# Optimization experiments

Measured on AMD Instinct MI355X. Metric: run time of the kernel, lower is better.

Reference implementation:

```python
import jax, jax.numpy as jnp
import numpy as np

T = 1024          # tokens (batch*seq, vLLM flattened layout)
D = 2048          # hidden_size
H = 16            # attention heads
HD = D // H       # head_dim = 128
E = 16            # num routed experts
K = 2             # top_k
IM = 1408         # moe_intermediate_size
IS = 5632         # shared_expert_intermediate_size
EPS = 1e-6
THETA = 10000.0


def setup_inputs() -> dict:
    key = jax.random.key(0)
    ks = jax.random.split(key, 14)
    s = 0.02  # weight scale
    n = jax.random.normal
    return {
        "positions": jnp.arange(T, dtype=jnp.int32),
        "hidden_states": n(ks[0], (T, D), jnp.float32),
        "ln1_w": 1.0 + s * n(ks[1], (D,), jnp.float32),
        "ln2_w": 1.0 + s * n(ks[2], (D,), jnp.float32),
        "qkv_w": s * n(ks[3], (D, 3 * H * HD), jnp.float32),
        "qkv_b": s * n(ks[4], (3 * H * HD,), jnp.float32),
        "o_w": s * n(ks[5], (H * HD, D), jnp.float32),
        "router_w": s * n(ks[6], (D, E), jnp.float32),
        "w_gate": s * n(ks[7], (E, D, IM), jnp.float32),
        "w_up": s * n(ks[8], (E, D, IM), jnp.float32),
        "w_down": s * n(ks[9], (E, IM, D), jnp.float32),
        "sh_gate_up": s * n(ks[10], (D, 2 * IS), jnp.float32),
        "sh_down": s * n(ks[11], (IS, D), jnp.float32),
        "sh_expert_gate": s * n(ks[12], (D, 1), jnp.float32),
    }


def _rmsnorm(x, w):
    var = jnp.mean(x * x, axis=-1, keepdims=True)
    return x * jax.lax.rsqrt(var + EPS) * w


def _rope(x, positions):
    # neox-style rotary: x [T, H, HD]
    half = HD // 2
    inv_freq = 1.0 / (THETA ** (jnp.arange(0, half, dtype=jnp.float32) / half * 1.0))
    inv_freq = 1.0 / (THETA ** (jnp.arange(0, HD, 2, dtype=jnp.float32) / HD))
    ang = positions.astype(jnp.float32)[:, None] * inv_freq  # [T, HD/2]
    cos = jnp.cos(ang)[:, None, :]
    sin = jnp.sin(ang)[:, None, :]
    x1, x2 = x[..., :half], x[..., half:]
    return jnp.concatenate([x1 * cos - x2 * sin, x2 * cos + x1 * sin], axis=-1)


def reference(positions, hidden_states, ln1_w, ln2_w, qkv_w, qkv_b, o_w,
              router_w, w_gate, w_up, w_down, sh_gate_up, sh_down,
              sh_expert_gate):
    # --- input RMSNorm (residual=None path) ---
    residual = hidden_states
    x = _rmsnorm(hidden_states, ln1_w)

    # --- self-attention: QKV + RoPE + causal SDPA + o_proj ---
    qkv = x @ qkv_w + qkv_b
    q, k, v = jnp.split(qkv, [H * HD, 2 * H * HD], axis=-1)
    q = _rope(q.reshape(T, H, HD), positions)
    k = _rope(k.reshape(T, H, HD), positions)
    v = v.reshape(T, H, HD)
    scale = HD ** -0.5
    scores = jnp.einsum('thd,shd->hts', q, k) * scale  # [H, T, T]
    causal = jnp.tril(jnp.ones((T, T), dtype=bool))
    scores = jnp.where(causal[None], scores, jnp.finfo(scores.dtype).min)
    attn = jax.nn.softmax(scores, axis=-1)
    ctx = jnp.einsum('hts,shd->thd', attn, v).reshape(T, H * HD)
    attn_out = ctx @ o_w

    # --- fused add + post-attention RMSNorm ---
    residual = residual + attn_out
    x = _rmsnorm(residual, ln2_w)

    # --- sparse MoE: router -> softmax -> top-k (renormalized) -> experts ---
    logits = x @ router_w                                    # [T, E]
    probs = jax.nn.softmax(logits.astype(jnp.float32), axis=-1)
    topv, topi = jax.lax.top_k(probs, K)                     # [T, K]
    topv = topv / jnp.sum(topv, axis=-1, keepdims=True)      # norm_topk_prob
    w = jnp.zeros((T, E), dtype=x.dtype).at[
        jnp.arange(T)[:, None], topi].set(topv.astype(x.dtype))
    g = jax.nn.silu(jnp.einsum('td,edi->tei', x, w_gate)) * \
        jnp.einsum('td,edi->tei', x, w_up)                   # [T, E, IM]
    moe_out = jnp.einsum('tei,eid,te->td', g, w_down, w)

    # --- shared expert with sigmoid gate ---
    gu = x @ sh_gate_up
    g2, u2 = jnp.split(gu, 2, axis=-1)
    shared = (jax.nn.silu(g2) * u2) @ sh_down
    shared = jax.nn.sigmoid(x @ sh_expert_gate) * shared

    hidden_states = moe_out + shared
    return hidden_states, residual
```

## Files before the change

### kernel.cpp

```cpp
#include <hip/hip_runtime.h>

constexpr int T_  = 1024;
constexpr int D_  = 2048;
constexpr int H_  = 16;
constexpr int HD_ = 128;
constexpr int E_  = 16;
constexpr int IM_ = 1408;
constexpr int IS_ = 5632;

typedef __attribute__((ext_vector_type(8))) short bf16x8;
typedef __attribute__((ext_vector_type(4))) short short4v;
typedef __attribute__((ext_vector_type(4))) float f32x4;

__device__ __forceinline__ short f2bf(float f){
  unsigned u = __builtin_bit_cast(unsigned, f);
  u += 0x7fffu + ((u >> 16) & 1u);
  return (short)(u >> 16);
}
__device__ __forceinline__ float bf2f(short s){
  unsigned u = ((unsigned)(unsigned short)s) << 16;
  return __builtin_bit_cast(float, u);
}
__device__ __forceinline__ unsigned cvtpk(float lo, float hi){
  unsigned r;
  asm("v_cvt_pk_bf16_f32 %0, %1, %2" : "=v"(r) : "v"(lo), "v"(hi));
  return r;
}
__device__ __forceinline__ float pk_lo(unsigned h){
  return __builtin_bit_cast(float, h << 16);
}
__device__ __forceinline__ float pk_hi(unsigned h){
  return __builtin_bit_cast(float, h & 0xffff0000u);
}
__device__ __forceinline__ f32x4 mfma16(bf16x8 a, bf16x8 b, f32x4 c){
  return __builtin_amdgcn_mfma_f32_16x16x32_bf16(a, b, c, 0, 0, 0);
}
__device__ __forceinline__ void split3(float f, short& h, short& m, short& l){
  h = f2bf(f); float r = f - bf2f(h);
  m = f2bf(r); l = f2bf(r - bf2f(m));
}
__device__ __forceinline__ void split2(float f, short& h, short& m){
  h = f2bf(f); m = f2bf(f - bf2f(h));
}
__device__ __forceinline__ uint4 mk4(unsigned a, unsigned b, unsigned c, unsigned d){
  uint4 r; r.x=a; r.y=b; r.z=c; r.w=d; return r;
}
#define LGKM0_BAR() do{ asm volatile("s_waitcnt lgkmcnt(0)" ::: "memory"); \
                        __builtin_amdgcn_s_barrier(); }while(0)

__global__ __launch_bounds__(256) void sctab_kernel(
    const int* __restrict__ pos, float* __restrict__ cst, float* __restrict__ snt)
{
  int idx = blockIdx.x * 256 + threadIdx.x;
  if (idx >= T_ * 64) return;
  int t = idx >> 6, i = idx & 63;
  float invf = (float)pow(10000.0, -(double)i / 64.0);
  float ang  = (float)pos[t] * invf;
  double s, c;
  sincos((double)ang, &s, &c);
  cst[idx] = (float)c; snt[idx] = (float)s;
}

__global__ __launch_bounds__(256) void rms_kernel(
    const float* __restrict__ x, const float* __restrict__ w,
    short* __restrict__ o0, short* __restrict__ o1, short* __restrict__ o2,
    short* __restrict__ ob, float* __restrict__ of)
{
  int t = blockIdx.x, tid = threadIdx.x;
  const float* xr = x + (size_t)t * D_;
  float4 va = ((const float4*)xr)[tid*2];
  float4 vb = ((const float4*)xr)[tid*2+1];
  float ss = va.x*va.x + va.y*va.y + va.z*va.z + va.w*va.w
           + vb.x*vb.x + vb.y*vb.y + vb.z*vb.z + vb.w*vb.w;
  for (int o = 32; o; o >>= 1) ss += __shfl_xor(ss, o, 64);
  __shared__ float red[4];
  int lane = tid & 63, wid = tid >> 6;
  if (lane == 0) red[wid] = ss;
  __syncthreads();
  ss = red[0] + red[1] + red[2] + red[3];
  float rs = 1.0f / sqrtf(ss * (1.0f/D_) + 1e-6f);
  float4 wa = ((const float4*)w)[tid*2];
  float4 wb = ((const float4*)w)[tid*2+1];
  float xv[8] = {va.x,va.y,va.z,va.w, vb.x,vb.y,vb.z,vb.w};
  float wv[8] = {wa.x,wa.y,wa.z,wa.w, wb.x,wb.y,wb.z,wb.w};
  size_t base = (size_t)t * D_ + tid*8;
  #pragma unroll
  for (int p = 0; p < 4; ++p){
    float f0 = xv[2*p]   * rs * wv[2*p];
    float f1 = xv[2*p+1] * rs * wv[2*p+1];
    if (o0){
      unsigned h = cvtpk(f0, f1);
      float r0 = f0 - pk_lo(h), r1 = f1 - pk_hi(h);
      unsigned m = cvtpk(r0, r1);
      unsigned l = cvtpk(r0 - pk_lo(m), r1 - pk_hi(m));
      *(unsigned*)&o0[base + 2*p] = h;
      *(unsigned*)&o1[base + 2*p] = m;
      *(unsigned*)&o2[base + 2*p] = l;
    }
    if (ob) *(unsigned*)&ob[base + 2*p] = cvtpk(f0, f1);
    if (of){ of[base + 2*p] = f0; of[base + 2*p + 1] = f1; }
  }
}

__global__ __launch_bounds__(256) void prepk_kernel(
    const float* __restrict__ qkv, const float* __restrict__ cst,
    const float* __restrict__ snt, short* __restrict__ Kp0, short* __restrict__ Kp1)
{
  int idx = blockIdx.x * 256 + threadIdx.x;
  int c = idx & 7, t = (idx >> 3) & (T_-1), h = idx >> 13;
  int d0 = c * 8;
  const float* kp = qkv + (size_t)t * (3*D_) + D_ + h*HD_;
  const float* cp = cst + t*64 + d0;
  const float* sp = snt + t*64 + d0;
  unsigned lh[4], ll[4], hh[4], hl[4];
  #pragma unroll
  for (int p = 0; p < 4; ++p){
    float xl0 = kp[d0+2*p],    xh0 = kp[d0+64+2*p];
    float xl1 = kp[d0+2*p+1],  xh1 = kp[d0+64+2*p+1];
    float cv0 = cp[2*p], sv0 = sp[2*p], cv1 = cp[2*p+1], sv1 = sp[2*p+1];
    float rl0 = xl0*cv0 - xh0*sv0, rh0 = xh0*cv0 + xl0*sv0;
    float rl1 = xl1*cv1 - xh1*sv1, rh1 = xh1*cv1 + xl1*sv1;
    unsigned a = cvtpk(rl0, rl1);
    ll[p] = cvtpk(rl0 - pk_lo(a), rl1 - pk_hi(a)); lh[p] = a;
    unsigned b = cvtpk(rh0, rh1);
    hl[p] = cvtpk(rh0 - pk_lo(b), rh1 - pk_hi(b)); hh[p] = b;
  }
  size_t ob = ((size_t)h*T_ + t) * HD_;
  *(uint4*)(Kp0 + ob + d0)      = mk4(lh[0],lh[1],lh[2],lh[3]);
  *(uint4*)(Kp0 + ob + 64 + d0) = mk4(hh[0],hh[1],hh[2],hh[3]);
  *(uint4*)(Kp1 + ob + d0)      = mk4(ll[0],ll[1],ll[2],ll[3]);
  *(uint4*)(Kp1 + ob + 64 + d0) = mk4(hl[0],hl[1],hl[2],hl[3]);
}

__global__ __launch_bounds__(256) void prepv_kernel(
    const float* __restrict__ qkv, short* __restrict__ Vp0, short* __restrict__ Vp1)
{
  __shared__ short Vl[2][128][72];
  int t0 = blockIdx.x * 64, h = blockIdx.y, tid = threadIdx.x;
  int r = tid >> 2, cq = (tid & 3) * 32;
  const float* src = qkv + (size_t)(t0+r) * (3*D_) + 2*D_ + h*HD_ + cq;
  #pragma unroll
  for (int jj = 0; jj < 8; ++jj){
    float4 v = *(const float4*)(src + jj*4);
    float vv[4] = {v.x, v.y, v.z, v.w};
    #pragma unroll
    for (int u = 0; u < 4; ++u){
      int d = cq + jj*4 + u;
      short a, b; split2(vv[u], a, b);
      Vl[0][d][r] = a; Vl[1][d][r] = b;
    }
  }
  __syncthreads();
  int d = tid >> 1, tc = (tid & 1) * 32;
  short* dst0 = Vp0 + ((size_t)h*HD_ + d) * T_ + t0 + tc;
  short* dst1 = Vp1 + ((size_t)h*HD_ + d) * T_ + t0 + tc;
  #pragma unroll
  for (int q = 0; q < 4; ++q){
    *(uint4*)(dst0 + q*8) = *(const uint4*)&Vl[0][d][tc + q*8];
    *(uint4*)(dst1 + q*8) = *(const uint4*)&Vl[1][d][tc + q*8];
  }
}

__global__ __launch_bounds__(256) void prepw_kernel(
    const float* __restrict__ w, short* __restrict__ P0, short* __restrict__ P1)
{
  __shared__ short L0[64][72], L1[64][72];
  int k0 = blockIdx.x * 64, n0 = blockIdx.y * 64;
  int tid = threadIdx.x;
  int r = tid >> 2, cq = (tid & 3) * 16;
  const float* src = w + (size_t)(k0 + r) * D_ + n0 + cq;
  #pragma unroll
  for (int q = 0; q < 4; ++q){
    float4 f = *(const float4*)(src + q*4);
    float fv[4] = {f.x, f.y, f.z, f.w};
    #pragma unroll
    for (int u = 0; u < 4; ++u){
      int n = cq + q*4 + u;
      short a, b; split2(fv[u], a, b);
      L0[n][r] = a; L1[n][r] = b;
    }
  }
  __syncthreads();
  int n = tid >> 2, kq = (tid & 3) * 16;
  short* d0 = P0 + (size_t)(n0 + n) * D_ + k0 + kq;
  short* d1 = P1 + (size_t)(n0 + n) * D_ + k0 + kq;
  *(uint4*)(d0)     = *(const uint4*)&L0[n][kq];
  *(uint4*)(d0 + 8) = *(const uint4*)&L0[n][kq + 8];
  *(uint4*)(d1)     = *(const uint4*)&L1[n][kq];
  *(uint4*)(d1 + 8) = *(const uint4*)&L1[n][kq + 8];
}

__global__ __launch_bounds__(128) void attn_kernel(
    const float* __restrict__ qkv,
    const float* __restrict__ cst, const float* __restrict__ snt,
    const short* __restrict__ Kp0, const short* __restrict__ Kp1,
    const short* __restrict__ Vp0, const short* __restrict__ Vp1,
    short* __restrict__ c0p, short* __restrict__ c1p, short* __restrict__ c2p)
{
  __shared__ __attribute__((aligned(16))) short Ks[2][2][32][128];
  __shared__ __attribute__((aligned(16))) short Vs[2][2][128][40];
  __shared__ __attribute__((aligned(16))) short Ps[3][2][16][40];

  const float SCALE = 0.08838834764831845f;
  const int QW = 3*D_;
  int h = blockIdx.x;
  int ys = blockIdx.y;
  int qt = (ys < 16) ? (ys*2) : ((31-ys)*2 + 1);
  int q0 = qt * 32;
  int tid = threadIdx.x, lane = tid & 63, wq = tid >> 6;
  int lr = lane & 15, kq8 = (lane >> 4) * 8, r4 = (lane >> 4) * 4;

  bf16x8 qfh[4], qfm[4], qfl[4];
  { int qrow = q0 + wq*16 + lr;
    const float* qp = qkv + (size_t)qrow * QW + h*HD_;
    const float* cp = cst + qrow*64;
    const float* sp = snt + qrow*64;
    float x[4][8], cs[2][8], sn[2][8], rot[4][8];
    for (int ks = 0; ks < 4; ++ks)
      for (int j = 0; j < 8; ++j) x[ks][j] = qp[ks*32 + kq8 + j];
    for (int hf = 0; hf < 2; ++hf)
      for (int j = 0; j < 8; ++j){
        cs[hf][j] = cp[hf*32 + kq8 + j];
        sn[hf][j] = sp[hf*32 + kq8 + j];
      }
    for (int j = 0; j < 8; ++j){
      rot[0][j] = x[0][j]*cs[0][j] - x[2][j]*sn[0][j];
      rot[1][j] = x[1][j]*cs[1][j] - x[3][j]*sn[1][j];
      rot[2][j] = x[2][j]*cs[0][j] + x[0][j]*sn[0][j];
      rot[3][j] = x[3][j]*cs[1][j] + x[1][j]*sn[1][j];
    }
    for (int ks = 0; ks < 4; ++ks)
      for (int j = 0; j < 8; ++j){
        short a, b, c; split3(rot[ks][j], a, b, c);
        qfh[ks][j] = a; qfm[ks][j] = b; qfl[ks][j] = c;
      }
  }

  f32x4 acc[8];
  for (int i = 0; i < 8; ++i) acc[i] = f32x4{0.f,0.f,0.f,0.f};
  float mrun[4] = {-1e30f,-1e30f,-1e30f,-1e30f};
  float lrun[4] = {0.f,0.f,0.f,0.f};

  int krow = tid >> 2, kc = (tid & 3) * 32;
  const short* kb0 = Kp0 + ((size_t)h*T_ + krow) * HD_ + kc;
  const short* kb1 = Kp1 + ((size_t)h*T_ + krow) * HD_ + kc;
  const short* vb0 = Vp0 + ((size_t)h*HD_ + tid) * T_;
  const short* vb1 = Vp1 + ((size_t)h*HD_ + tid) * T_;
  int xr = (krow & 7) * 8;

  uint4 kr0[4], kr1[4], vr0[4], vr1[4];
  auto LOAD = [&](int it){
    size_t ko = (size_t)it * 32 * HD_;
    const uint4* p0 = (const uint4*)(kb0 + ko);
    const uint4* p1 = (const uint4*)(kb1 + ko);
    #pragma unroll
    for (int g = 0; g < 4; ++g){ kr0[g] = p0[g]; kr1[g] = p1[g]; }
    const uint4* q0p = (const uint4*)(vb0 + it*32);
    const uint4* q1p = (const uint4*)(vb1 + it*32);
    #pragma unroll
    for (int g = 0; g < 4; ++g){ vr0[g] = q0p[g]; vr1[g] = q1p[g]; }
  };
  auto STORE = [&](int buf){
    #pragma unroll
    for (int g = 0; g < 4; ++g){
      int col = (kc + 8*g) ^ xr;
      *(uint4*)&Ks[buf][0][krow][col] = kr0[g];
      *(uint4*)&Ks[buf][1][krow][col] = kr1[g];
    }
    #pragma unroll
    for (int g = 0; g < 4; ++g){
      *(uint4*)&Vs[buf][0][tid][g*8] = vr0[g];
      *(uint4*)&Vs[buf][1][tid][g*8] = vr1[g];
    }
  };

  int nt = qt + 1;
  LOAD(0); STORE(0);
  if (nt > 1) LOAD(1);
  LGKM0_BAR();

  int cur = 0;
  for (int it = 0; it < nt; ++it){
    if (it + 1 < nt){
      STORE(cur ^ 1);
      if (it + 2 < nt) LOAD(it + 2);
    }
    int kv0 = it * 32;
    int xl = (lr & 7) * 8;
    f32x4 s0 = f32x4{0.f,0.f,0.f,0.f}, s1 = f32x4{0.f,0.f,0.f,0.f};
    #pragma unroll
    for (int ks = 0; ks < 4; ++ks){
      int col = (ks*32 + kq8) ^ xl;
      bf16x8 b0h = *(const bf16x8*)&Ks[cur][0][lr][col];
      bf16x8 b0m = *(const bf16x8*)&Ks[cur][1][lr][col];
      bf16x8 b1h = *(const bf16x8*)&Ks[cur][0][16+lr][col];
      bf16x8 b1m = *(const bf16x8*)&Ks[cur][1][16+lr][col];
      s0 = mfma16(qfh[ks], b0h, s0); s0 = mfma16(qfh[ks], b0m, s0);
      s0 = mfma16(qfm[ks], b0h, s0); s0 = mfma16(qfm[ks], b0m, s0);
      s0 = mfma16(qfl[ks], b0h, s0);
      s1 = mfma16(qfh[ks], b1h, s1); s1 = mfma16(qfh[ks], b1m, s1);
      s1 = mfma16(qfm[ks], b1h, s1); s1 = mfma16(qfm[ks], b1m, s1);
      s1 = mfma16(qfl[ks], b1h, s1);
    }
    float pm[2][4]; float alpha[4];
    for (int r = 0; r < 4; ++r){
      int qr = q0 + wq*16 + r4 + r;
      float x0 = s0[r]*SCALE, x1 = s1[r]*SCALE;
      if (kv0 + lr > qr)      x0 = -1e30f;
      if (kv0 + 16 + lr > qr) x1 = -1e30f;
      float mt_ = fmaxf(x0, x1);
      mt_ = fmaxf(mt_, __shfl_xor(mt_, 1, 64));
      mt_ = fmaxf(mt_, __shfl_xor(mt_, 2, 64));
      mt_ = fmaxf(mt_, __shfl_xor(mt_, 4, 64));
      mt_ = fmaxf(mt_, __shfl_xor(mt_, 8, 64));
      float mn = fmaxf(mrun[r], mt_);
      float p0 = __expf(x0 - mn), p1 = __expf(x1 - mn);
      pm[0][r] = p0; pm[1][r] = p1;
      float ls = p0 + p1;
      ls += __shfl_xor(ls, 1, 64); ls += __shfl_xor(ls, 2, 64);
      ls += __shfl_xor(ls, 4, 64); ls += __shfl_xor(ls, 8, 64);
      alpha[r] = __expf(mrun[r] - mn);
      lrun[r] = lrun[r]*alpha[r] + ls;
      mrun[r] = mn;
    }
    for (int dt = 0; dt < 8; ++dt){
      f32x4 a = acc[dt];
      a[0]*=alpha[0]; a[1]*=alpha[1]; a[2]*=alpha[2]; a[3]*=alpha[3];
      acc[dt] = a;
    }
    for (int nn = 0; nn < 2; ++nn)
      for (int r = 0; r < 4; ++r){
        short a, b, c; split3(pm[nn][r], a, b, c);
        Ps[0][wq][r4+r][nn*16+lr] = a;
        Ps[1][wq][r4+r][nn*16+lr] = b;
        Ps[2][wq][r4+r][nn*16+lr] = c;
      }
    bf16x8 pah = *(const bf16x8*)&Ps[0][wq][lr][kq8];
    bf16x8 pam = *(const bf16x8*)&Ps[1][wq][lr][kq8];
    bf16x8 pal = *(const bf16x8*)&Ps[2][wq][lr][kq8];
    #pragma unroll
    for (int dt = 0; dt < 8; ++dt){
      bf16x8 vbh = *(const bf16x8*)&Vs[cur][0][dt*16+lr][kq8];
      bf16x8 vbm = *(const bf16x8*)&Vs[cur][1][dt*16+lr][kq8];
      acc[dt] = mfma16(pah, vbh, acc[dt]);
      acc[dt] = mfma16(pah, vbm, acc[dt]);
      acc[dt] = mfma16(pam, vbh, acc[dt]);
      acc[dt] = mfma16(pam, vbm, acc[dt]);
      acc[dt] = mfma16(pal, vbh, acc[dt]);
    }
    LGKM0_BAR();
    cur ^= 1;
  }
  for (int dt = 0; dt < 8; ++dt)
    for (int r = 0; r < 4; ++r){
      int qr = q0 + wq*16 + r4 + r;
      float o = acc[dt][r] / lrun[r];
      size_t ix = (size_t)qr * D_ + h*HD_ + dt*16 + lr;
      short a, b, c; split3(o, a, b, c);
      c0p[ix] = a; c1p[ix] = b; c2p[ix] = c;
    }
}

enum { M_QKV = 0, M_OPROJ = 1 };

template<int MODE>
__global__ __launch_bounds__(256) void gemm3_kernel(
    const short* __restrict__ A0, const short* __restrict__ A1, const short* __restrict__ A2,
    const float* __restrict__ Bw,
    const short* __restrict__ Bp0, const short* __restrict__ Bp1,
    const float* __restrict__ bias, const float* __restrict__ addsrc,
    float* __restrict__ outF,
    int K, int lda, int ldb, int ldo)
{
  __shared__ __attribute__((aligned(16))) short As[2][3][64][40];
  __shared__ __attribute__((aligned(16))) short Bs[2][2][64][40];

  int m0 = blockIdx.y * 64, n0 = blockIdx.x * 64;
  int tid = threadIdx.x, lane = tid & 63, wid = tid >> 6;
  int wm = wid >> 1, wn = wid & 1;
  int lr = lane & 15, kq8 = (lane >> 4) * 8;

  f32x4 acc[2][2];
  for (int i = 0; i < 2; ++i)
    for (int j = 0; j < 2; ++j) acc[i][j] = f32x4{0.f,0.f,0.f,0.f};

  int arow = tid >> 2, ac = (tid & 3) * 8;
  const short* aP0 = A0 + (size_t)(m0 + arow) * lda + ac;
  const short* aP1 = A1 + (size_t)(m0 + arow) * lda + ac;
  const short* aP2 = A2 + (size_t)(m0 + arow) * lda + ac;
  int bn = tid & 63, bk0 = (tid >> 6) * 8;
  const float* bP  = Bw  ? (Bw + n0 + bn) : nullptr;
  const short* bq0 = Bp0 ? (Bp0 + (size_t)(n0 + bn) * K) : nullptr;
  const short* bq1 = Bp1 ? (Bp1 + (size_t)(n0 + bn) * K) : nullptr;

  uint4 ar0_0, ar1_0, ar2_0, ar0_1, ar1_1, ar2_1;
  float br_0[8], br_1[8];
  uint4 pb0_0, pb1_0, pb0_1, pb1_1;

  auto LOAD0 = [&](int kt){
    ar0_0 = *(const uint4*)(aP0 + kt*32);
    ar1_0 = *(const uint4*)(aP1 + kt*32);
    ar2_0 = *(const uint4*)(aP2 + kt*32);
    if constexpr (MODE == M_QKV){
      const float* p = bP + (size_t)(kt*32 + bk0) * ldb;
      #pragma unroll
      for (int j = 0; j < 8; ++j) br_0[j] = p[(size_t)j * ldb];
    } else {
      pb0_0 = *(const uint4*)(bq0 + kt*32 + bk0);
      pb1_0 = *(const uint4*)(bq1 + kt*32 + bk0);
    }
  };
  auto LOAD1 = [&](int kt){
    ar0_1 = *(const uint4*)(aP0 + kt*32);
    ar1_1 = *(const uint4*)(aP1 + kt*32);
    ar2_1 = *(const uint4*)(aP2 + kt*32);
    if constexpr (MODE == M_QKV){
      const float* p = bP + (size_t)(kt*32 + bk0) * ldb;
      #pragma unroll
      for (int j = 0; j < 8; ++j) br_1[j] = p[(size_t)j * ldb];
    } else {
      pb0_1 = *(const uint4*)(bq0 + kt*32 + bk0);
      pb1_1 = *(const uint4*)(bq1 + kt*32 + bk0);
    }
  };
  auto STORE0 = [&](int buf){
    *(uint4*)&As[buf][0][arow][ac] = ar0_0;
    *(uint4*)&As[buf][1][arow][ac] = ar1_0;
    *(uint4*)&As[buf][2][arow][ac] = ar2_0;
    if constexpr (MODE == M_QKV){
      unsigned hh[4], mm[4];
      #pragma unroll
      for (int p = 0; p < 4; ++p){
        unsigned h = cvtpk(br_0[2*p], br_0[2*p+1]);
        mm[p] = cvtpk(br_0[2*p] - pk_lo(h), br_0[2*p+1] - pk_hi(h));
        hh[p] = h;
      }
      *(uint4*)&Bs[buf][0][bn][bk0] = mk4(hh[0],hh[1],hh[2],hh[3]);
      *(uint4*)&Bs[buf][1][bn][bk0] = mk4(mm[0],mm[1],mm[2],mm[3]);
    } else {
      *(uint4*)&Bs[buf][0][bn][bk0] = pb0_0;
      *(uint4*)&Bs[buf][1][bn][bk0] = pb1_0;
    }
  };
  auto STORE1 = [&](int buf){
    *(uint4*)&As[buf][0][arow][ac] = ar0_1;
    *(uint4*)&As[buf][1][arow][ac] = ar1_1;
    *(uint4*)&As[buf][2][arow][ac] = ar2_1;
    if constexpr (MODE == M_QKV){
      unsigned hh[4], mm[4];
      #pragma unroll
      for (int p = 0; p < 4; ++p){
        unsigned h = cvtpk(br_1[2*p], br_1[2*p+1]);
        mm[p] = cvtpk(br_1[2*p] - pk_lo(h), br_1[2*p+1] - pk_hi(h));
        hh[p] = h;
      }
      *(uint4*)&Bs[buf][0][bn][bk0] = mk4(hh[0],hh[1],hh[2],hh[3]);
      *(uint4*)&Bs[buf][1][bn][bk0] = mk4(mm[0],mm[1],mm[2],mm[3]);
    } else {
      *(uint4*)&Bs[buf][0][bn][bk0] = pb0_1;
      *(uint4*)&Bs[buf][1][bn][bk0] = pb1_1;
    }
  };
  auto COMPUTE = [&](int cur){
    bf16x8 aH[2], aM[2], aL[2];
    #pragma unroll
    for (int mt = 0; mt < 2; ++mt){
      aH[mt] = *(const bf16x8*)&As[cur][0][wm*32 + mt*16 + lr][kq8];
      aM[mt] = *(const bf16x8*)&As[cur][1][wm*32 + mt*16 + lr][kq8];
      aL[mt] = *(const bf16x8*)&As[cur][2][wm*32 + mt*16 + lr][kq8];
    }
    #pragma unroll
    for (int nt = 0; nt < 2; ++nt){
      bf16x8 bH = *(const bf16x8*)&Bs[cur][0][wn*32 + nt*16 + lr][kq8];
      bf16x8 bM = *(const bf16x8*)&Bs[cur][1][wn*32 + nt*16 + lr][kq8];
      #pragma unroll
      for (int mt = 0; mt < 2; ++mt){
        f32x4 a = acc[mt][nt];
        a = mfma16(aH[mt], bH, a);
        a = mfma16(aH[mt], bM, a);
        a = mfma16(aM[mt], bH, a);
        a = mfma16(aM[mt], bM, a);
        a = mfma16(aL[mt], bH, a);
        acc[mt][nt] = a;
      }
    }
  };

  int NK = K / 32;
  LOAD0(0); LOAD1(1);
  STORE0(0);
  LOAD0(2);
  LGKM0_BAR();

  int cur = 0;
  for (int kt = 0; kt < NK; kt += 2){
    if (kt + 1 < NK) STORE1(cur ^ 1);
    if (kt + 3 < NK) LOAD1(kt + 3);
    COMPUTE(cur);
    LGKM0_BAR();
    cur ^= 1;
    if (kt + 1 < NK){
      if (kt + 2 < NK) STORE0(cur ^ 1);
      if (kt + 4 < NK) LOAD0(kt + 4);
      COMPUTE(cur);
      LGKM0_BAR();
      cur ^= 1;
    }
  }

  for (int mt = 0; mt < 2; ++mt)
    for (int nt = 0; nt < 2; ++nt)
      for (int r = 0; r < 4; ++r){
        int mrow = m0 + wm*32 + mt*16 + (lane >> 4)*4 + r;
        int col  = n0 + wn*32 + nt*16 + lr;
        float v = acc[mt][nt][r];
        if constexpr (MODE == M_QKV){
          outF[(size_t)mrow * ldo + col] = v + bias[col];
        } else {
          outF[(size_t)mrow * ldo + col] = v + addsrc[(size_t)mrow * ldo + col];
        }
      }
}

__global__ __launch_bounds__(256) void gu_kernel(
    const short* __restrict__ x2b,
    const float* __restrict__ w_gate, const float* __restrict__ w_up,
    const float* __restrict__ sh_gu,
    short* __restrict__ gbuf, short* __restrict__ sbuf,
    const int* __restrict__ perm, const int* __restrict__ offE,
    const int* __restrict__ cntE)
{
  __shared__ __attribute__((aligned(16))) short As[2][128][40];
  __shared__ __attribute__((aligned(16))) short Bs[2][2][64][40];

  int z = blockIdx.z;
  bool SH = (z == E_);
  int N    = SH ? IS_ : IM_;
  int n0 = blockIdx.x * 64;
  if (n0 >= N) return;
  int mcnt  = SH ? T_ : cntE[z];
  int mbase = SH ? 0  : offE[z];
  int m0 = blockIdx.y * 128;
  if (m0 >= mcnt) return;
  int ldb = SH ? 2*IS_ : IM_;
  int ldo = SH ? IS_   : IM_;
  const float* Bg = SH ? sh_gu         : (w_gate + (size_t)z * D_ * IM_);
  const float* Bu = SH ? (sh_gu + IS_) : (w_up   + (size_t)z * D_ * IM_);
  short* outB = SH ? sbuf : gbuf;

  int tid = threadIdx.x, lane = tid & 63, wid = tid >> 6;
  int wm = wid >> 1, wn = wid & 1;
  int lr = lane & 15, kq8 = (lane >> 4) * 8;

  f32x4 acc0[4][2], acc1[4][2];
  #pragma unroll
  for (int i = 0; i < 4; ++i)
    for (int j = 0; j < 2; ++j){
      acc0[i][j] = f32x4{0.f,0.f,0.f,0.f};
      acc1[i][j] = f32x4{0.f,0.f,0.f,0.f};
    }

  int arow = tid >> 1, acol = (tid & 1) * 16;
  int aRowIdx;
  { int mr = m0 + arow;
    int mc = (mr < mcnt) ? mr : 0;
    aRowIdx = SH ? mc : perm[mbase + mc];
  }
  const short* aP = x2b + (size_t)aRowIdx * D_;

  int bn_ = tid & 63, bkq = (tid >> 6) * 8;
  const float* bP0 = Bg + n0 + bn_;
  const float* bP1 = Bu + n0 + bn_;

  uint4 arA_0, arB_0, arA_1, arB_1;
  float br0_0[8], br1_0[8], br0_1[8], br1_1[8];

  auto LOAD0 = [&](int kt){
    const uint4* s = (const uint4*)(aP + kt*32 + acol);
    arA_0 = s[0]; arB_0 = s[1];
    const float* p0 = bP0 + (size_t)(kt*32 + bkq) * ldb;
    const float* p1 = bP1 + (size_t)(kt*32 + bkq) * ldb;
    #pragma unroll
    for (int j = 0; j < 8; ++j){ br0_0[j] = p0[(size_t)j * ldb]; br1_0[j] = p1[(size_t)j * ldb]; }
  };
  auto LOAD1 = [&](int kt){
    const uint4* s = (const uint4*)(aP + kt*32 + acol);
    arA_1 = s[0]; arB_1 = s[1];
    const float* p0 = bP0 + (size_t)(kt*32 + bkq) * ldb;
    const float* p1 = bP1 + (size_t)(kt*32 + bkq) * ldb;
    #pragma unroll
    for (int j = 0; j < 8; ++j){ br0_1[j] = p0[(size_t)j * ldb]; br1_1[j] = p1[(size_t)j * ldb]; }
  };
  auto STORE0 = [&](int buf){
    *(uint4*)&As[buf][arow][acol]   = arA_0;
    *(uint4*)&As[buf][arow][acol+8] = arB_0;
    unsigned v0[4], v1[4];
    #pragma unroll
    for (int p = 0; p < 4; ++p){
      v0[p] = cvtpk(br0_0[2*p], br0_0[2*p+1]);
      v1[p] = cvtpk(br1_0[2*p], br1_0[2*p+1]);
    }
    *(uint4*)&Bs[buf][0][bn_][bkq] = mk4(v0[0],v0[1],v0[2],v0[3]);
    *(uint4*)&Bs[buf][1][bn_][bkq] = mk4(v1[0],v1[1],v1[2],v1[3]);
  };
  auto STORE1 = [&](int buf){
    *(uint4*)&As[buf][arow][acol]   = arA_1;
    *(uint4*)&As[buf][arow][acol+8] = arB_1;
    unsigned v0[4], v1[4];
    #pragma unroll
    for (int p = 0; p < 4; ++p){
      v0[p] = cvtpk(br0_1[2*p], br0_1[2*p+1]);
      v1[p] = cvtpk(br1_1[2*p], br1_1[2*p+1]);
    }
    *(uint4*)&Bs[buf][0][bn_][bkq] = mk4(v0[0],v0[1],v0[2],v0[3]);
    *(uint4*)&Bs[buf][1][bn_][bkq] = mk4(v1[0],v1[1],v1[2],v1[3]);
  };
  auto COMPUTE = [&](int cur){
    bf16x8 a[4];
    #pragma unroll
    for (int mt = 0; mt < 4; ++mt)
      a[mt] = *(const bf16x8*)&As[cur][wm*64 + mt*16 + lr][kq8];
    #pragma unroll
    for (int nt = 0; nt < 2; ++nt){
      int nrow = wn*32 + nt*16 + lr;
      bf16x8 b0 = *(const bf16x8*)&Bs[cur][0][nrow][kq8];
      bf16x8 b1 = *(const bf16x8*)&Bs[cur][1][nrow][kq8];
      #pragma unroll
      for (int mt = 0; mt < 4; ++mt){
        acc0[mt][nt] = mfma16(a[mt], b0, acc0[mt][nt]);
        acc1[mt][nt] = mfma16(a[mt], b1, acc1[mt][nt]);
      }
    }
  };

  constexpr int NK = D_ / 32;
  LOAD0(0); LOAD1(1);
  STORE0(0);
  LOAD0(2);
  LGKM0_BAR();

  int cur = 0;
  for (int kt = 0; kt < NK; kt += 2){
    if (kt + 1 < NK) STORE1(cur ^ 1);
    if (kt + 3 < NK) LOAD1(kt + 3);
    COMPUTE(cur);
    LGKM0_BAR();
    cur ^= 1;
    if (kt + 2 < NK) STORE0(cur ^ 1);
    if (kt + 4 < NK) LOAD0(kt + 4);
    COMPUTE(cur);
    LGKM0_BAR();
    cur ^= 1;
  }

  for (int mt = 0; mt < 4; ++mt)
    for (int nt = 0; nt < 2; ++nt)
      for (int r = 0; r < 4; ++r){
        int mrow = m0 + wm*64 + mt*16 + (lane >> 4)*4 + r;
        if (mrow >= mcnt) continue;
        int col = n0 + wn*32 + nt*16 + lr;
        float v = acc0[mt][nt][r];
        float u = acc1[mt][nt][r];
        float sv = v / (1.f + __expf(-v)) * u;
        outB[(size_t)(mbase + mrow) * ldo + col] = f2bf(sv);
      }
}

__global__ __launch_bounds__(256) void dn_kernel(
    const short* __restrict__ gbuf, const short* __restrict__ sbuf,
    const float* __restrict__ w_down, const float* __restrict__ sh_down,
    float* __restrict__ outF,
    const int* __restrict__ perm, const int* __restrict__ offE,
    const int* __restrict__ cntE, const float* __restrict__ wgt,
    const float* __restrict__ sig)
{
  __shared__ __attribute__((aligned(16))) short As[2][128][40];
  __shared__ __attribute__((aligned(16))) short Bs[2][64][40];

  int z = blockIdx.z;
  bool SH = (z == E_);
  int K = SH ? IS_ : IM_;
  int mcnt  = SH ? T_ : cntE[z];
  int mbase = SH ? 0  : offE[z];
  int m0 = blockIdx.y * 128;
  if (m0 >= mcnt) return;
  int n0 = blockIdx.x * 64;
  const float* Bq = SH ? sh_down : (w_down + (size_t)z * IM_ * D_);
  const short* Ab = SH ? sbuf : gbuf;

  int tid = threadIdx.x, lane = tid & 63, wid = tid >> 6;
  int wm = wid >> 1, wn = wid & 1;
  int lr = lane & 15, kq8 = (lane >> 4) * 8;

  f32x4 acc0[4][2];
  #pragma unroll
  for (int i = 0; i < 4; ++i)
    for (int j = 0; j < 2; ++j) acc0[i][j] = f32x4{0.f,0.f,0.f,0.f};

  int arow = tid >> 1, acol = (tid & 1) * 16;
  int mr = m0 + arow;
  int mc = (mr < mcnt) ? mr : 0;
  const short* aP = Ab + (size_t)(SH ? mc : (mbase + mc)) * K;

  int bn_ = tid & 63, bkq = (tid >> 6) * 8;
  const float* bP0 = Bq + n0 + bn_;

  uint4 arA_0, arB_0, arA_1, arB_1;
  float br_0[8], br_1[8];

  auto LOAD0 = [&](int kt){
    const uint4* s = (const uint4*)(aP + kt*32 + acol);
    arA_0 = s[0]; arB_0 = s[1];
    const float* p0 = bP0 + (size_t)(kt*32 + bkq) * D_;
    #pragma unroll
    for (int j = 0; j < 8; ++j) br_0[j] = p0[(size_t)j * D_];
  };
  auto LOAD1 = [&](int kt){
    const uint4* s = (const uint4*)(aP + kt*32 + acol);
    arA_1 = s[0]; arB_1 = s[1];
    const float* p0 = bP0 + (size_t)(kt*32 + bkq) * D_;
    #pragma unroll
    for (int j = 0; j < 8; ++j) br_1[j] = p0[(size_t)j * D_];
  };
  auto STORE0 = [&](int buf){
    *(uint4*)&As[buf][arow][acol]   = arA_0;
    *(uint4*)&As[buf][arow][acol+8] = arB_0;
    unsigned v0[4];
    #pragma unroll
    for (int p = 0; p < 4; ++p) v0[p] = cvtpk(br_0[2*p], br_0[2*p+1]);
    *(uint4*)&Bs[buf][bn_][bkq] = mk4(v0[0],v0[1],v0[2],v0[3]);
  };
  auto STORE1 = [&](int buf){
    *(uint4*)&As[buf][arow][acol]   = arA_1;
    *(uint4*)&As[buf][arow][acol+8] = arB_1;
    unsigned v0[4];
    #pragma unroll
    for (int p = 0; p < 4; ++p) v0[p] = cvtpk(br_1[2*p], br_1[2*p+1]);
    *(uint4*)&Bs[buf][bn_][bkq] = mk4(v0[0],v0[1],v0[2],v0[3]);
  };
  auto COMPUTE = [&](int cur){
    bf16x8 a[4];
    #pragma unroll
    for (int mt = 0; mt < 4; ++mt)
      a[mt] = *(const bf16x8*)&As[cur][wm*64 + mt*16 + lr][kq8];
    #pragma unroll
    for (int nt = 0; nt < 2; ++nt){
      bf16x8 b0 = *(const bf16x8*)&Bs[cur][wn*32 + nt*16 + lr][kq8];
      #pragma unroll
      for (int mt = 0; mt < 4; ++mt)
        acc0[mt][nt] = mfma16(a[mt], b0, acc0[mt][nt]);
    }
  };

  int NK = K / 32;
  LOAD0(0); LOAD1(1);
  STORE0(0);
  LOAD0(2);
  LGKM0_BAR();

  int cur = 0;
  for (int kt = 0; kt < NK; kt += 2){
    if (kt + 1 < NK) STORE1(cur ^ 1);
    if (kt + 3 < NK) LOAD1(kt + 3);
    COMPUTE(cur);
    LGKM0_BAR();
    cur ^= 1;
    if (kt + 2 < NK) STORE0(cur ^ 1);
    if (kt + 4 < NK) LOAD0(kt + 4);
    COMPUTE(cur);
    LGKM0_BAR();
    cur ^= 1;
  }

  for (int mt = 0; mt < 4; ++mt)
    for (int nt = 0; nt < 2; ++nt)
      for (int r = 0; r < 4; ++r){
        int mrow = m0 + wm*64 + mt*16 + (lane >> 4)*4 + r;
        if (mrow >= mcnt) continue;
        int col = n0 + wn*32 + nt*16 + lr;
        float v = acc0[mt][nt][r];
        if (SH){
          atomicAdd(&outF[(size_t)mrow * D_ + col], sig[mrow] * v);
        } else {
          int tk = perm[mbase + mrow];
          atomicAdd(&outF[(size_t)tk * D_ + col], v * wgt[mbase + mrow]);
        }
      }
}

__global__ __launch_bounds__(256) void router_kernel(
    const float* __restrict__ x2f, const float* __restrict__ rw,
    const float* __restrict__ seg, int* __restrict__ te, float* __restrict__ tw,
    float* __restrict__ sig, int* __restrict__ cnt)
{
  int t = blockIdx.x, tid = threadIdx.x, lane = tid & 63, w = tid >> 6;
  const float* xr = x2f + (size_t)t * D_;
  float a0 = 0.f, a1 = 0.f, a2 = 0.f, a3 = 0.f, ag = 0.f;
  for (int j = 0; j < 32; ++j){
    int d = lane + 64*j;
    float xv = xr[d];
    const float* rp = rw + (size_t)d * E_ + w*4;
    a0 += xv * rp[0]; a1 += xv * rp[1]; a2 += xv * rp[2]; a3 += xv * rp[3];
    ag += xv * seg[d];
  }
  for (int o = 32; o; o >>= 1){
    a0 += __shfl_xor(a0, o, 64); a1 += __shfl_xor(a1, o, 64);
    a2 += __shfl_xor(a2, o, 64); a3 += __shfl_xor(a3, o, 64);
    ag += __shfl_xor(ag, o, 64);
  }
  __shared__ float lg[16];
  __shared__ float sgv;
  if (lane == 0){
    lg[w*4+0] = a0; lg[w*4+1] = a1; lg[w*4+2] = a2; lg[w*4+3] = a3;
    if (w == 0) sgv = ag;
  }
  __syncthreads();
  if (tid == 0){
    int e0 = 0; float v0 = lg[0];
    for (int ee = 1; ee < 16; ++ee) if (lg[ee] > v0){ v0 = lg[ee]; e0 = ee; }
    int e1 = -1; float v1 = -3e38f;
    for (int ee = 0; ee < 16; ++ee){
      if (ee == e0) continue;
      if (lg[ee] > v1){ v1 = lg[ee]; e1 = ee; }
    }
    float w0 = 1.f / (1.f + expf(v1 - v0));
    te[2*t] = e0; te[2*t+1] = e1;
    tw[2*t] = w0; tw[2*t+1] = 1.f - w0;
    atomicAdd(&cnt[e0], 1); atomicAdd(&cnt[e1], 1);
    sig[t] = 1.f / (1.f + expf(-sgv));
  }
}

__global__ void prefix_kernel(const int* __restrict__ cnt, int* __restrict__ offE,
                              int* __restrict__ cursor)
{
  if (threadIdx.x == 0){
    int s = 0;
    for (int e = 0; e < 16; ++e){ offE[e] = s; s += cnt[e]; }
  }
  if (threadIdx.x < 16) cursor[threadIdx.x] = 0;
}

__global__ __launch_bounds__(256) void scatter_kernel(
    const int* __restrict__ te, const float* __restrict__ tw,
    const int* __restrict__ offE, int* __restrict__ cursor,
    int* __restrict__ perm, float* __restrict__ wgt)
{
  int t = blockIdx.x * 256 + threadIdx.x;
  if (t >= T_) return;
  for (int i = 0; i < 2; ++i){
    int e = te[2*t + i];
    int pos = offE[e] + atomicAdd(&cursor[e], 1);
    perm[pos] = t; wgt[pos] = tw[2*t + i];
  }
}

extern "C" void kernel_launch(void* const* d_in, const int* in_sizes, int n_in,
                              void* d_out, int out_size, void* d_ws, size_t ws_size,
                              hipStream_t stream)
{
  const int*   positions = (const int*)  d_in[0];
  const float* hidden    = (const float*)d_in[1];
  const float* ln1       = (const float*)d_in[2];
  const float* ln2       = (const float*)d_in[3];
  const float* qkv_w     = (const float*)d_in[4];
  const float* qkv_b     = (const float*)d_in[5];
  const float* o_w       = (const float*)d_in[6];
  const float* router_w  = (const float*)d_in[7];
  const float* w_gate    = (const float*)d_in[8];
  const float* w_up      = (const float*)d_in[9];
  const float* w_down    = (const float*)d_in[10];
  const float* sh_gu     = (const float*)d_in[11];
  const float* sh_down   = (const float*)d_in[12];
  const float* sh_eg     = (const float*)d_in[13];

  float* out_hidden = (float*)d_out;
  float* out_resid  = (float*)d_out + (size_t)T_ * D_;

  char* wp = (char*)d_ws;
  auto alloc = [&](size_t b){ char* p = wp; wp += (b + 255) & ~(size_t)255; return p; };

  float* qkv  = (float*)alloc((size_t)T_ * 3*D_ * 4);
  short* x1h  = (short*)alloc((size_t)T_ * D_ * 2);
  short* x1m  = (short*)alloc((size_t)T_ * D_ * 2);
  short* x1l  = (short*)alloc((size_t)T_ * D_ * 2);
  short* Kp0  = (short*)alloc((size_t)T_ * D_ * 2);
  short* Kp1  = (short*)alloc((size_t)T_ * D_ * 2);
  short* Vp0  = (short*)alloc((size_t)T_ * D_ * 2);
  short* Vp1  = (short*)alloc((size_t)T_ * D_ * 2);
  float* cst  = (float*)alloc((size_t)T_ * 64 * 4);
  float* snt  = (float*)alloc((size_t)T_ * 64 * 4);
  int*   te   = (int*)  alloc(2*T_*4);
  float* tw   = (float*)alloc(2*T_*4);
  float* sig  = (float*)alloc(T_*4);
  int*   cnt    = (int*)alloc(256);
  int*   offE   = (int*)alloc(256);
  int*   cursor = (int*)alloc(256);
  int*   perm = (int*)  alloc(2*T_*4);
  float* wgt  = (float*)alloc(2*T_*4);

  short* ctxh = x1h;
  short* ctxm = x1m;
  short* ctxl = x1l;
  float* x2f  = qkv;
  short* sbuf = (short*)((char*)qkv + (size_t)8388608);
  short* gbuf = (short*)x1h;
  short* x2b  = (short*)((char*)x1h + (size_t)5767168);
  short* Wo0  = Kp0;
  short* Wo1  = Vp0;

  hipMemsetAsync(cnt, 0, 64, stream);
  hipMemsetAsync(out_hidden, 0, (size_t)T_ * D_ * 4, stream);

  sctab_kernel<<<(T_*64)/256, 256, 0, stream>>>(positions, cst, snt);

  rms_kernel<<<T_, 256, 0, stream>>>(hidden, ln1, x1h, x1m, x1l, nullptr, nullptr);

  gemm3_kernel<M_QKV><<<dim3(96, 16), 256, 0, stream>>>(
      x1h, x1m, x1l, qkv_w, nullptr, nullptr, qkv_b, nullptr, qkv,
      D_, D_, 3*D_, 3*D_);

  prepk_kernel<<<(T_*H_*8)/256, 256, 0, stream>>>(qkv, cst, snt, Kp0, Kp1);
  prepv_kernel<<<dim3(16, 16), 256, 0, stream>>>(qkv, Vp0, Vp1);

  attn_kernel<<<dim3(16, 32), 128, 0, stream>>>(
      qkv, cst, snt, Kp0, Kp1, Vp0, Vp1, ctxh, ctxm, ctxl);

  prepw_kernel<<<dim3(32, 32), 256, 0, stream>>>(o_w, Wo0, Wo1);

  gemm3_kernel<M_OPROJ><<<dim3(32, 16), 256, 0, stream>>>(
      ctxh, ctxm, ctxl, nullptr, Wo0, Wo1, nullptr, hidden, out_resid,
      D_, D_, D_, D_);

  rms_kernel<<<T_, 256, 0, stream>>>(out_resid, ln2, nullptr, nullptr, nullptr, x2b, x2f);

  router_kernel<<<T_, 256, 0, stream>>>(x2f, router_w, sh_eg, te, tw, sig, cnt);
  prefix_kernel<<<1, 64, 0, stream>>>(cnt, offE, cursor);
  scatter_kernel<<<4, 256, 0, stream>>>(te, tw, offE, cursor, perm, wgt);

  gu_kernel<<<dim3(88, 8, 17), 256, 0, stream>>>(
      x2b, w_gate, w_up, sh_gu, gbuf, sbuf, perm, offE, cnt);

  dn_kernel<<<dim3(32, 8, 17), 256, 0, stream>>>(
      gbuf, sbuf, w_down, sh_down, out_hidden, perm, offE, cnt, wgt, sig);

  (void)in_sizes; (void)n_in; (void)out_size; (void)ws_size;
}
```

Before: 965.6 us.

## Split down-projection K across blocks and shorten A-operand prefetch distance

The down-projection kernel now splits its reduction dimension: each routed expert is handled by two blocks over halves of IM, and the shared expert by four blocks over quarters of IS, with partial results combined through the existing atomicAdd epilogue. The grid z grows from 17 to 36 so more blocks can run at once and the long shared-expert tail is broken up. Across the GEMM kernels, the activation (A) tile prefetch now runs one stage ahead instead of two and uses a single register set, while the weight (B) tile keeps two-stage prefetch. This is meant to cut register pressure and raise occupancy, at the cost of more atomic traffic and less latency hiding on A loads.

After: 924.9 us. -4.2%, faster.

```diff
diff --git a/kernel.cpp b/kernel.cpp
--- a/kernel.cpp
+++ b/kernel.cpp
@@ -393,14 +393,16 @@
   const short* bq0 = Bp0 ? (Bp0 + (size_t)(n0 + bn) * K) : nullptr;
   const short* bq1 = Bp1 ? (Bp1 + (size_t)(n0 + bn) * K) : nullptr;
 
-  uint4 ar0_0, ar1_0, ar2_0, ar0_1, ar1_1, ar2_1;
+  uint4 ar0, ar1, ar2;
   float br_0[8], br_1[8];
   uint4 pb0_0, pb1_0, pb0_1, pb1_1;
 
-  auto LOAD0 = [&](int kt){
-    ar0_0 = *(const uint4*)(aP0 + kt*32);
-    ar1_0 = *(const uint4*)(aP1 + kt*32);
-    ar2_0 = *(const uint4*)(aP2 + kt*32);
+  auto LOADA = [&](int kt){
+    ar0 = *(const uint4*)(aP0 + kt*32);
+    ar1 = *(const uint4*)(aP1 + kt*32);
+    ar2 = *(const uint4*)(aP2 + kt*32);
+  };
+  auto LOADB0 = [&](int kt){
     if constexpr (MODE == M_QKV){
       const float* p = bP + (size_t)(kt*32 + bk0) * ldb;
       #pragma unroll
@@ -410,10 +412,7 @@
       pb1_0 = *(const uint4*)(bq1 + kt*32 + bk0);
     }
   };
-  auto LOAD1 = [&](int kt){
-    ar0_1 = *(const uint4*)(aP0 + kt*32);
-    ar1_1 = *(const uint4*)(aP1 + kt*32);
-    ar2_1 = *(const uint4*)(aP2 + kt*32);
+  auto LOADB1 = [&](int kt){
     if constexpr (MODE == M_QKV){
       const float* p = bP + (size_t)(kt*32 + bk0) * ldb;
       #pragma unroll
@@ -423,10 +422,12 @@
       pb1_1 = *(const uint4*)(bq1 + kt*32 + bk0);
     }
   };
-  auto STORE0 = [&](int buf){
-    *(uint4*)&As[buf][0][arow][ac] = ar0_0;
-    *(uint4*)&As[buf][1][arow][ac] = ar1_0;
-    *(uint4*)&As[buf][2][arow][ac] = ar2_0;
+  auto STOREA = [&](int buf){
+    *(uint4*)&As[buf][0][arow][ac] = ar0;
+    *(uint4*)&As[buf][1][arow][ac] = ar1;
+    *(uint4*)&As[buf][2][arow][ac] = ar2;
+  };
+  auto STOREB0 = [&](int buf){
     if constexpr (MODE == M_QKV){
       unsigned hh[4], mm[4];
       #pragma unroll
@@ -442,10 +443,7 @@
       *(uint4*)&Bs[buf][1][bn][bk0] = pb1_0;
     }
   };
-  auto STORE1 = [&](int buf){
-    *(uint4*)&As[buf][0][arow][ac] = ar0_1;
-    *(uint4*)&As[buf][1][arow][ac] = ar1_1;
-    *(uint4*)&As[buf][2][arow][ac] = ar2_1;
+  auto STOREB1 = [&](int buf){
     if constexpr (MODE == M_QKV){
       unsigned hh[4], mm[4];
       #pragma unroll
@@ -487,21 +485,27 @@
   };
 
   int NK = K / 32;
-  LOAD0(0); LOAD1(1);
-  STORE0(0);
-  LOAD0(2);
+  LOADA(0); LOADB0(0);
+  STOREA(0); STOREB0(0);
+  LOADA(1); LOADB1(1); LOADB0(2);
   LGKM0_BAR();
 
   int cur = 0;
   for (int kt = 0; kt < NK; kt += 2){
-    if (kt + 1 < NK) STORE1(cur ^ 1);
-    if (kt + 3 < NK) LOAD1(kt + 3);
+    if (kt + 1 < NK){
+      STOREA(cur ^ 1); STOREB1(cur ^ 1);
+      if (kt + 2 < NK) LOADA(kt + 2);
+      if (kt + 3 < NK) LOADB1(kt + 3);
+    }
     COMPUTE(cur);
     LGKM0_BAR();
     cur ^= 1;
+    if (kt + 2 < NK){
+      STOREA(cur ^ 1); STOREB0(cur ^ 1);
+      if (kt + 3 < NK) LOADA(kt + 3);
+      if (kt + 4 < NK) LOADB0(kt + 4);
+    }
     if (kt + 1 < NK){
-      if (kt + 2 < NK) STORE0(cur ^ 1);
-      if (kt + 4 < NK) LOAD0(kt + 4);
       COMPUTE(cur);
       LGKM0_BAR();
       cur ^= 1;
@@ -572,28 +576,31 @@
   const float* bP0 = Bg + n0 + bn_;
   const float* bP1 = Bu + n0 + bn_;
 
-  uint4 arA_0, arB_0, arA_1, arB_1;
-  float br0_0[8], br1_0[8], br0_1[8], br1_1[8];
-
-  auto LOAD0 = [&](int kt){
+  uint4 arA, arB;
+  float br0_0[8], br1_0[8];
+  float br0_1[8], br1_1[8];
+
+  auto LOADA = [&](int kt){
     const uint4* s = (const uint4*)(aP + kt*32 + acol);
-    arA_0 = s[0]; arB_0 = s[1];
+    arA = s[0]; arB = s[1];
+  };
+  auto LOADB0 = [&](int kt){
     const float* p0 = bP0 + (size_t)(kt*32 + bkq) * ldb;
     const float* p1 = bP1 + (size_t)(kt*32 + bkq) * ldb;
     #pragma unroll
     for (int j = 0; j < 8; ++j){ br0_0[j] = p0[(size_t)j * ldb]; br1_0[j] = p1[(size_t)j * ldb]; }
   };
-  auto LOAD1 = [&](int kt){
-    const uint4* s = (const uint4*)(aP + kt*32 + acol);
-    arA_1 = s[0]; arB_1 = s[1];
+  auto LOADB1 = [&](int kt){
     const float* p0 = bP0 + (size_t)(kt*32 + bkq) * ldb;
     const float* p1 = bP1 + (size_t)(kt*32 + bkq) * ldb;
     #pragma unroll
     for (int j = 0; j < 8; ++j){ br0_1[j] = p0[(size_t)j * ldb]; br1_1[j] = p1[(size_t)j * ldb]; }
   };
-  auto STORE0 = [&](int buf){
-    *(uint4*)&As[buf][arow][acol]   = arA_0;
-    *(uint4*)&As[buf][arow][acol+8] = arB_0;
+  auto STOREA = [&](int buf){
+    *(uint4*)&As[buf][arow][acol]   = arA;
+    *(uint4*)&As[buf][arow][acol+8] = arB;
+  };
+  auto STOREB0 = [&](int buf){
     unsigned v0[4], v1[4];
     #pragma unroll
     for (int p = 0; p < 4; ++p){
@@ -603,9 +610,7 @@
     *(uint4*)&Bs[buf][0][bn_][bkq] = mk4(v0[0],v0[1],v0[2],v0[3]);
     *(uint4*)&Bs[buf][1][bn_][bkq] = mk4(v1[0],v1[1],v1[2],v1[3]);
   };
-  auto STORE1 = [&](int buf){
-    *(uint4*)&As[buf][arow][acol]   = arA_1;
-    *(uint4*)&As[buf][arow][acol+8] = arB_1;
+  auto STOREB1 = [&](int buf){
     unsigned v0[4], v1[4];
     #pragma unroll
     for (int p = 0; p < 4; ++p){
@@ -634,23 +639,31 @@
   };
 
   constexpr int NK = D_ / 32;
-  LOAD0(0); LOAD1(1);
-  STORE0(0);
-  LOAD0(2);
+  LOADA(0); LOADB0(0);
+  STOREA(0); STOREB0(0);
+  LOADA(1); LOADB1(1); LOADB0(2);
   LGKM0_BAR();
 
   int cur = 0;
   for (int kt = 0; kt < NK; kt += 2){
-    if (kt + 1 < NK) STORE1(cur ^ 1);
-    if (kt + 3 < NK) LOAD1(kt + 3);
+    if (kt + 1 < NK){
+      STOREA(cur ^ 1); STOREB1(cur ^ 1);
+      if (kt + 2 < NK) LOADA(kt + 2);
+      if (kt + 3 < NK) LOADB1(kt + 3);
+    }
     COMPUTE(cur);
     LGKM0_BAR();
     cur ^= 1;
-    if (kt + 2 < NK) STORE0(cur ^ 1);
-    if (kt + 4 < NK) LOAD0(kt + 4);
-    COMPUTE(cur);
-    LGKM0_BAR();
-    cur ^= 1;
+    if (kt + 2 < NK){
+      STOREA(cur ^ 1); STOREB0(cur ^ 1);
+      if (kt + 3 < NK) LOADA(kt + 3);
+      if (kt + 4 < NK) LOADB0(kt + 4);
+    }
+    if (kt + 1 < NK){
+      COMPUTE(cur);
+      LGKM0_BAR();
+      cur ^= 1;
+    }
   }
 
   for (int mt = 0; mt < 4; ++mt)
@@ -678,15 +691,24 @@
   __shared__ __attribute__((aligned(16))) short Bs[2][64][40];
 
   int z = blockIdx.z;
-  bool SH = (z == E_);
-  int K = SH ? IS_ : IM_;
-  int mcnt  = SH ? T_ : cntE[z];
-  int mbase = SH ? 0  : offE[z];
+  bool SH = (z >= 2*E_);
+  int K, kbase, NK, mcnt, mbase;
+  const float* Bq;
+  const short* Ab;
+  if (SH){
+    int q = z - 2*E_;
+    K = IS_; kbase = q * (IS_/4); NK = (IS_/4)/32;
+    mcnt = T_; mbase = 0;
+    Bq = sh_down; Ab = sbuf;
+  } else {
+    int e = z >> 1, half = z & 1;
+    K = IM_; kbase = half * (IM_/2); NK = (IM_/2)/32;
+    mcnt = cntE[e]; mbase = offE[e];
+    Bq = w_down + (size_t)e * IM_ * D_; Ab = gbuf;
+  }
   int m0 = blockIdx.y * 128;
   if (m0 >= mcnt) return;
   int n0 = blockIdx.x * 64;
-  const float* Bq = SH ? sh_down : (w_down + (size_t)z * IM_ * D_);
-  const short* Ab = SH ? sbuf : gbuf;
 
   int tid = threadIdx.x, lane = tid & 63, wid = tid >> 6;
   int wm = wid >> 1, wn = wid & 1;
@@ -700,39 +722,39 @@
   int arow = tid >> 1, acol = (tid & 1) * 16;
   int mr = m0 + arow;
   int mc = (mr < mcnt) ? mr : 0;
-  const short* aP = Ab + (size_t)(SH ? mc : (mbase + mc)) * K;
+  const short* aP = Ab + (size_t)(SH ? mc : (mbase + mc)) * K + kbase;
 
   int bn_ = tid & 63, bkq = (tid >> 6) * 8;
-  const float* bP0 = Bq + n0 + bn_;
-
-  uint4 arA_0, arB_0, arA_1, arB_1;
+  const float* bP0 = Bq + (size_t)kbase * D_ + n0 + bn_;
+
+  uint4 arA, arB;
   float br_0[8], br_1[8];
 
-  auto LOAD0 = [&](int kt){
+  auto LOADA = [&](int kt){
     const uint4* s = (const uint4*)(aP + kt*32 + acol);
-    arA_0 = s[0]; arB_0 = s[1];
+    arA = s[0]; arB = s[1];
+  };
+  auto LOADB0 = [&](int kt){
     const float* p0 = bP0 + (size_t)(kt*32 + bkq) * D_;
     #pragma unroll
     for (int j = 0; j < 8; ++j) br_0[j] = p0[(size_t)j * D_];
   };
-  auto LOAD1 = [&](int kt){
-    const uint4* s = (const uint4*)(aP + kt*32 + acol);
-    arA_1 = s[0]; arB_1 = s[1];
+  auto LOADB1 = [&](int kt){
     const float* p0 = bP0 + (size_t)(kt*32 + bkq) * D_;
     #pragma unroll
     for (int j = 0; j < 8; ++j) br_1[j] = p0[(size_t)j * D_];
   };
-  auto STORE0 = [&](int buf){
-    *(uint4*)&As[buf][arow][acol]   = arA_0;
-    *(uint4*)&As[buf][arow][acol+8] = arB_0;
+  auto STOREA = [&](int buf){
+    *(uint4*)&As[buf][arow][acol]   = arA;
+    *(uint4*)&As[buf][arow][acol+8] = arB;
+  };
+  auto STOREB0 = [&](int buf){
     unsigned v0[4];
     #pragma unroll
     for (int p = 0; p < 4; ++p) v0[p] = cvtpk(br_0[2*p], br_0[2*p+1]);
     *(uint4*)&Bs[buf][bn_][bkq] = mk4(v0[0],v0[1],v0[2],v0[3]);
   };
-  auto STORE1 = [&](int buf){
-    *(uint4*)&As[buf][arow][acol]   = arA_1;
-    *(uint4*)&As[buf][arow][acol+8] = arB_1;
+  auto STOREB1 = [&](int buf){
     unsigned v0[4];
     #pragma unroll
     for (int p = 0; p < 4; ++p) v0[p] = cvtpk(br_1[2*p], br_1[2*p+1]);
@@ -752,24 +774,31 @@
     }
   };
 
-  int NK = K / 32;
-  LOAD0(0); LOAD1(1);
-  STORE0(0);
-  LOAD0(2);
+  LOADA(0); LOADB0(0);
+  STOREA(0); STOREB0(0);
+  LOADA(1); LOADB1(1); LOADB0(2);
   LGKM0_BAR();
 
   int cur = 0;
   for (int kt = 0; kt < NK; kt += 2){
-    if (kt + 1 < NK) STORE1(cur ^ 1);
-    if (kt + 3 < NK) LOAD1(kt + 3);
+    if (kt + 1 < NK){
+      STOREA(cur ^ 1); STOREB1(cur ^ 1);
+      if (kt + 2 < NK) LOADA(kt + 2);
+      if (kt + 3 < NK) LOADB1(kt + 3);
+    }
     COMPUTE(cur);
     LGKM0_BAR();
     cur ^= 1;
-    if (kt + 2 < NK) STORE0(cur ^ 1);
-    if (kt + 4 < NK) LOAD0(kt + 4);
-    COMPUTE(cur);
-    LGKM0_BAR();
-    cur ^= 1;
+    if (kt + 2 < NK){
+      STOREA(cur ^ 1); STOREB0(cur ^ 1);
+      if (kt + 3 < NK) LOADA(kt + 3);
+      if (kt + 4 < NK) LOADB0(kt + 4);
+    }
+    if (kt + 1 < NK){
+      COMPUTE(cur);
+      LGKM0_BAR();
+      cur ^= 1;
+    }
   }
 
   for (int mt = 0; mt < 4; ++mt)
@@ -941,7 +970,7 @@
   gu_kernel<<<dim3(88, 8, 17), 256, 0, stream>>>(
       x2b, w_gate, w_up, sh_gu, gbuf, sbuf, perm, offE, cnt);
 
-  dn_kernel<<<dim3(32, 8, 17), 256, 0, stream>>>(
+  dn_kernel<<<dim3(32, 8, 36), 256, 0, stream>>>(
       gbuf, sbuf, w_down, sh_down, out_hidden, perm, offE, cnt, wgt, sig);
 
   (void)in_sizes; (void)n_in; (void)out_size; (void)ws_size;
```
